# Kernel tuning notes

Hardware: AMD Instinct MI355X
Metric: run time of the kernel (lower is better)

## Reference

```python
import jax, jax.numpy as jnp
import numpy as np

B, C, E = 4, 2048, 1024
H, D = 16, 64  # num_heads, head_size

def setup_inputs() -> dict:
    key = jax.random.key(0)
    kx, kk, kq, kv, ko = jax.random.split(key, 5)
    s = 1.0 / np.sqrt(E)
    so = 1.0 / np.sqrt(H * D)
    return {
        "x": jax.random.normal(kx, (B, C, E), dtype=jnp.float32),
        "Wk": jax.random.uniform(kk, (H * D, E), jnp.float32, -s, s),
        "Wq": jax.random.uniform(kq, (H * D, E), jnp.float32, -s, s),
        "Wv": jax.random.uniform(kv, (H * D, E), jnp.float32, -s, s),
        "Wo": jax.random.uniform(ko, (E, H * D), jnp.float32, -so, so),
    }

def reference(x, Wk, Wq, Wv, Wo):
    b, c, e = x.shape
    # projections -> [B, H, C, D]
    def proj(W):
        return (x @ W.T).reshape(b, c, H, D).transpose(0, 2, 1, 3)
    k = proj(Wk)
    q = proj(Wq)
    v = proj(Wv)
    # scores [B, H, C, C]; mask applied before scaling (as in source; -inf*scale = -inf)
    sa = jnp.einsum("bhqd,bhkd->bhqk", q, k)
    mask = ~jnp.tril(jnp.ones((c, c), dtype=bool))  # True above diagonal
    masked = jnp.where(mask, -jnp.inf, sa)
    scale = 1.0 / np.sqrt(D)
    attn = jax.nn.softmax(masked * scale, axis=-1)
    out = jnp.einsum("bhqk,bhkd->bhqd", attn, v)  # [B, H, C, D]
    flat = out.transpose(0, 2, 1, 3).reshape(b, c, H * D)
    return flat @ Wo.T
```

## Files before the change

### kernel.cpp

```cpp
#include <hip/hip_runtime.h>
#include <hip/hip_bf16.h>

typedef __bf16 bf16x8 __attribute__((ext_vector_type(8)));
typedef __bf16 bf16x4 __attribute__((ext_vector_type(4)));
typedef float f32x4 __attribute__((ext_vector_type(4)));

#define NEG_INF (-__builtin_inff())

__global__ void cvt_f32_bf16(const float* __restrict__ src, __bf16* __restrict__ dst, int n) {
    int idx = blockIdx.x * blockDim.x + threadIdx.x;
    int stride = gridDim.x * blockDim.x;
    for (int i = idx * 4; i < n; i += stride * 4) {
        float4 v = *(const float4*)(src + i);
        bf16x4 o;
        o[0] = (__bf16)v.x; o[1] = (__bf16)v.y; o[2] = (__bf16)v.z; o[3] = (__bf16)v.w;
        *(bf16x4*)(dst + i) = o;
    }
}

template <int MODE>
__launch_bounds__(256, 2)
__global__ void gemm_bt(const __bf16* __restrict__ A, const __bf16* __restrict__ Bm,
                        void* __restrict__ Out, int M, int N, int K) {
    __shared__ __bf16 As[128][72];
    __shared__ __bf16 Bs[128][72];
    const int tid = threadIdx.x;
    const int w = tid >> 6, lane = tid & 63;
    const int lr = lane & 15, lg = lane >> 4;
    const int m0 = blockIdx.y * 128, n0 = blockIdx.x * 128;
    const int wm0 = (w >> 1) * 64, wn0 = (w & 1) * 64;

    f32x4 acc[4][4] = {};

    const int srow = tid >> 3;
    const int scol = (tid & 7) * 8;
    const __bf16* Ap = A + (size_t)(m0 + srow) * K + scol;
    const __bf16* Bp = Bm + (size_t)(n0 + srow) * K + scol;

    bf16x8 ar[4], br[4];
#pragma unroll
    for (int i = 0; i < 4; ++i) {
        ar[i] = *(const bf16x8*)(Ap + (size_t)i * 32 * K);
        br[i] = *(const bf16x8*)(Bp + (size_t)i * 32 * K);
    }

    const int nt = K >> 6;
    for (int t = 0; t < nt; ++t) {
        __syncthreads();
#pragma unroll
        for (int i = 0; i < 4; ++i) {
            *(bf16x8*)&As[srow + i * 32][scol] = ar[i];
            *(bf16x8*)&Bs[srow + i * 32][scol] = br[i];
        }
        __syncthreads();
        if (t + 1 < nt) {
            const __bf16* Ap2 = Ap + (size_t)(t + 1) * 64;
            const __bf16* Bp2 = Bp + (size_t)(t + 1) * 64;
#pragma unroll
            for (int i = 0; i < 4; ++i) {
                ar[i] = *(const bf16x8*)(Ap2 + (size_t)i * 32 * K);
                br[i] = *(const bf16x8*)(Bp2 + (size_t)i * 32 * K);
            }
        }
#pragma unroll
        for (int kk = 0; kk < 2; ++kk) {
            bf16x8 af[4], bf[4];
#pragma unroll
            for (int mi = 0; mi < 4; ++mi)
                af[mi] = *(const bf16x8*)&As[wm0 + mi * 16 + lr][kk * 32 + lg * 8];
#pragma unroll
            for (int ni = 0; ni < 4; ++ni)
                bf[ni] = *(const bf16x8*)&Bs[wn0 + ni * 16 + lr][kk * 32 + lg * 8];
#pragma unroll
            for (int mi = 0; mi < 4; ++mi)
#pragma unroll
                for (int ni = 0; ni < 4; ++ni)
                    acc[mi][ni] = __builtin_amdgcn_mfma_f32_16x16x32_bf16(
                        af[mi], bf[ni], acc[mi][ni], 0, 0, 0);
        }
    }

#pragma unroll
    for (int mi = 0; mi < 4; ++mi)
#pragma unroll
        for (int ni = 0; ni < 4; ++ni)
#pragma unroll
            for (int r = 0; r < 4; ++r) {
                int m = m0 + wm0 + mi * 16 + lg * 4 + r;
                int n = n0 + wn0 + ni * 16 + lr;
                float v = acc[mi][ni][r];
                if (MODE == 0) {
                    int proj = n >> 10, nn = n & 1023;
                    int h = nn >> 6, d = nn & 63;
                    int bb = m >> 11, c = m & 2047;
                    if (proj == 2) {
                        ((__bf16*)Out)[(size_t)2 * 8388608 +
                                       ((size_t)((bb * 16 + h) * 64 + d)) * 2048 + c] = (__bf16)v;
                    } else {
                        float scale = (proj == 0) ? 0.125f : 1.0f;
                        ((__bf16*)Out)[(size_t)proj * 8388608 +
                                       ((size_t)(bb * 16 + h) * 2048 + c) * 64 + d] =
                            (__bf16)(v * scale);
                    }
                } else {
                    ((float*)Out)[(size_t)m * N + n] = v;
                }
            }
}

__device__ __forceinline__ unsigned swz(unsigned d) {
    return d ^ (((d >> 7) & 7) << 4);
}

__launch_bounds__(256, 4)
__global__ void attn_fwd(const __bf16* __restrict__ Q, const __bf16* __restrict__ K,
                         const __bf16* __restrict__ Vt, __bf16* __restrict__ Aout) {
    __shared__ char smem[40960];
    const int id = blockIdx.x;
    const int vid = (id & 7) * 128 + (id >> 3);
    const int bh = vid >> 4, pr = vid & 15;
    const int w = threadIdx.x >> 6, lane = threadIdx.x & 63;
    const int lr = lane & 15, lg = lane >> 4;
    const char* Kb  = (const char*)(K  + (size_t)bh * 2048 * 64);
    const char* Vtb = (const char*)(Vt + (size_t)bh * 64 * 2048);
    const __bf16* Qb = Q + (size_t)bh * 2048 * 64;
    const int b = bh >> 4, h = bh & 15;
    char* Pb = smem + 32768 + w * 2048;

    for (int pass = 0; pass < 2; ++pass) {
        const int qt = pass ? pr : 31 - pr;
        const int q0 = qt * 64 + w * 16;
        const int nt = qt + 1;

        bf16x8 qf[2];
#pragma unroll
        for (int kk = 0; kk < 2; ++kk)
            qf[kk] = *(const bf16x8*)&Qb[(size_t)(q0 + lr) * 64 + kk * 32 + lg * 8];

        f32x4 o[4] = {};
        float m = NEG_INF, l = 0.f;

        __syncthreads();
        {
            char* kd = smem;
            char* vd = smem + 16384;
#pragma unroll
            for (int i = 0; i < 2; ++i) {
                unsigned c = (unsigned)(w * 2 + i);
                unsigned d = c * 1024 + (unsigned)lane * 16;
                unsigned bs = swz(d);
                __builtin_amdgcn_global_load_lds(
                    (const __attribute__((address_space(1))) void*)(Kb + bs),
                    (__attribute__((address_space(3))) void*)(kd + c * 1024), 16, 0, 0);
                unsigned row = bs >> 7, colb = bs & 127;
                __builtin_amdgcn_global_load_lds(
                    (const __attribute__((address_space(1))) void*)(Vtb + (size_t)row * 4096 + colb),
                    (__attribute__((address_space(3))) void*)(vd + c * 1024), 16, 0, 0);
            }
        }

        for (int t = 0; t < nt; ++t) {
            __syncthreads();
            if (t + 1 < nt) {
                char* kd = smem + ((t + 1) & 1) * 8192;
                char* vd = smem + 16384 + ((t + 1) & 1) * 8192;
#pragma unroll
                for (int i = 0; i < 2; ++i) {
                    unsigned c = (unsigned)(w * 2 + i);
                    unsigned d = c * 1024 + (unsigned)lane * 16;
                    unsigned bs = swz(d);
                    __builtin_amdgcn_global_load_lds(
                        (const __attribute__((address_space(1))) void*)(Kb + (size_t)(t + 1) * 8192 + bs),
                        (__attribute__((address_space(3))) void*)(kd + c * 1024), 16, 0, 0);
                    unsigned row = bs >> 7, colb = bs & 127;
                    __builtin_amdgcn_global_load_lds(
                        (const __attribute__((address_space(1))) void*)(Vtb + (size_t)row * 4096 +
                                                                       (size_t)(t + 1) * 128 + colb),
                        (__attribute__((address_space(3))) void*)(vd + c * 1024), 16, 0, 0);
                }
            }
            const char* Ks = smem + (t & 1) * 8192;
            const char* Vs = smem + 16384 + (t & 1) * 8192;
            const int k0 = t * 64;

            f32x4 s[4] = {};
#pragma unroll
            for (int kk = 0; kk < 2; ++kk)
#pragma unroll
                for (int sub = 0; sub < 4; ++sub) {
                    bf16x8 kf = *(const bf16x8*)(Ks + swz((unsigned)((sub * 16 + lr) * 128 + kk * 64 + lg * 16)));
                    s[sub] = __builtin_amdgcn_mfma_f32_16x16x32_bf16(kf, qf[kk], s[sub], 0, 0, 0);
                }
            if (t == qt) {
#pragma unroll
                for (int sub = 0; sub < 4; ++sub)
#pragma unroll
                    for (int r = 0; r < 4; ++r)
                        if (k0 + sub * 16 + lg * 4 + r > q0 + lr) s[sub][r] = NEG_INF;
            }
            float mloc = NEG_INF;
#pragma unroll
            for (int sub = 0; sub < 4; ++sub)
#pragma unroll
                for (int r = 0; r < 4; ++r) mloc = fmaxf(mloc, s[sub][r]);
            mloc = fmaxf(mloc, __shfl_xor(mloc, 16));
            mloc = fmaxf(mloc, __shfl_xor(mloc, 32));
            float mnew = fmaxf(m, mloc);
            float alpha = __expf(m - mnew);
            float rs = 0.f;
#pragma unroll
            for (int sub = 0; sub < 4; ++sub)
#pragma unroll
                for (int r = 0; r < 4; ++r) {
                    float p = __expf(s[sub][r] - mnew);
                    s[sub][r] = p;
                    rs += p;
                }
            rs += __shfl_xor(rs, 16);
            rs += __shfl_xor(rs, 32);
            l = l * alpha + rs;
            m = mnew;
#pragma unroll
            for (int ni = 0; ni < 4; ++ni) o[ni] *= alpha;

#pragma unroll
            for (int sub = 0; sub < 4; ++sub) {
                bf16x4 pk;
#pragma unroll
                for (int r = 0; r < 4; ++r) pk[r] = (__bf16)s[sub][r];
                *(bf16x4*)(Pb + swz((unsigned)(lr * 128 + sub * 32 + lg * 8))) = pk;
            }
            bf16x8 pfr[2];
#pragma unroll
            for (int kk = 0; kk < 2; ++kk)
                pfr[kk] = *(const bf16x8*)(Pb + swz((unsigned)(lr * 128 + kk * 64 + lg * 16)));

#pragma unroll
            for (int kk = 0; kk < 2; ++kk)
#pragma unroll
                for (int ni = 0; ni < 4; ++ni) {
                    bf16x8 vf = *(const bf16x8*)(Vs + swz((unsigned)((ni * 16 + lr) * 128 + kk * 64 + lg * 16)));
                    o[ni] = __builtin_amdgcn_mfma_f32_16x16x32_bf16(vf, pfr[kk], o[ni], 0, 0, 0);
                }
        }

        float rinv = 1.0f / l;
#pragma unroll
        for (int ni = 0; ni < 4; ++ni) {
            bf16x4 ov;
#pragma unroll
            for (int r = 0; r < 4; ++r) ov[r] = (__bf16)(o[ni][r] * rinv);
            *(bf16x4*)&Aout[((size_t)b * 2048 + q0 + lr) * 1024 + h * 64 + ni * 16 + lg * 4] = ov;
        }
    }
}

extern "C" void kernel_launch(void* const* d_in, const int* in_sizes, int n_in,
                              void* d_out, int out_size, void* d_ws, size_t ws_size,
                              hipStream_t stream) {
    const float* x  = (const float*)d_in[0];
    const float* Wk = (const float*)d_in[1];
    const float* Wq = (const float*)d_in[2];
    const float* Wv = (const float*)d_in[3];
    const float* Wo = (const float*)d_in[4];

    char* ws = (char*)d_ws;
    __bf16* xb   = (__bf16*)(ws);
    __bf16* wqkv = (__bf16*)(ws + 16777216);
    __bf16* wo_b = (__bf16*)(ws + 23068672);
    __bf16* qkv  = (__bf16*)(ws + 25165824);
    __bf16* aout = (__bf16*)(ws + 75497472);
    float* out = (float*)d_out;

    cvt_f32_bf16<<<2048, 256, 0, stream>>>(x, xb, 8388608);
    cvt_f32_bf16<<<1024, 256, 0, stream>>>(Wq, wqkv, 1048576);
    cvt_f32_bf16<<<1024, 256, 0, stream>>>(Wk, wqkv + 1048576, 1048576);
    cvt_f32_bf16<<<1024, 256, 0, stream>>>(Wv, wqkv + 2097152, 1048576);
    cvt_f32_bf16<<<1024, 256, 0, stream>>>(Wo, wo_b, 1048576);

    gemm_bt<0><<<dim3(24, 64), 256, 0, stream>>>(xb, wqkv, qkv, 8192, 3072, 1024);
    attn_fwd<<<dim3(1024), 256, 0, stream>>>(qkv, qkv + 8388608, qkv + 16777216, aout);
    gemm_bt<1><<<dim3(8, 64), 256, 0, stream>>>(aout, wo_b, out, 8192, 1024, 1024);
}
```

Before: 192.1 us.

## Rewrite projection GEMMs as 256x256 tiles with async LDS loads and ping-pong

Replaces the 128x128 register-staged GEMM with a 512-thread, 256x256-tile kernel. It loads global memory directly into swizzled LDS through global_load_lds, double-buffers the K tiles, interleaves quarter-tile MFMA phases with barriers and setprio, and remaps block IDs into 8 groups for cache locality. The aim is more reuse per block, hiding load latency behind MFMA work, and avoiding LDS bank conflicts. In exchange it uses 128KB of LDS per block and launches far fewer blocks (128 for the output GEMM), which may underfill the 256 CUs.

```diff
diff --git a/kernel.cpp b/kernel.cpp
--- a/kernel.cpp
+++ b/kernel.cpp
@@ -6,6 +6,8 @@
 typedef float f32x4 __attribute__((ext_vector_type(4)));
 
 #define NEG_INF (-__builtin_inff())
+
+#define BAR() do { asm volatile("" ::: "memory"); __builtin_amdgcn_s_barrier(); asm volatile("" ::: "memory"); } while (0)
 
 __global__ void cvt_f32_bf16(const float* __restrict__ src, __bf16* __restrict__ dst, int n) {
     int idx = blockIdx.x * blockDim.x + threadIdx.x;
@@ -19,75 +21,118 @@
 }
 
 template <int MODE>
-__launch_bounds__(256, 2)
-__global__ void gemm_bt(const __bf16* __restrict__ A, const __bf16* __restrict__ Bm,
-                        void* __restrict__ Out, int M, int N, int K) {
-    __shared__ __bf16 As[128][72];
-    __shared__ __bf16 Bs[128][72];
+__launch_bounds__(512, 2)
+__global__ void gemm8(const __bf16* __restrict__ A, const __bf16* __restrict__ Bm,
+                      void* __restrict__ Out, int M, int N, int K) {
+    __shared__ __align__(1024) char smem[131072];
     const int tid = threadIdx.x;
     const int w = tid >> 6, lane = tid & 63;
     const int lr = lane & 15, lg = lane >> 4;
-    const int m0 = blockIdx.y * 128, n0 = blockIdx.x * 128;
-    const int wm0 = (w >> 1) * 64, wn0 = (w & 1) * 64;
-
-    f32x4 acc[4][4] = {};
-
-    const int srow = tid >> 3;
-    const int scol = (tid & 7) * 8;
-    const __bf16* Ap = A + (size_t)(m0 + srow) * K + scol;
-    const __bf16* Bp = Bm + (size_t)(n0 + srow) * K + scol;
-
-    bf16x8 ar[4], br[4];
-#pragma unroll
-    for (int i = 0; i < 4; ++i) {
-        ar[i] = *(const bf16x8*)(Ap + (size_t)i * 32 * K);
-        br[i] = *(const bf16x8*)(Bp + (size_t)i * 32 * K);
+    const int wr = w >> 2, wc = w & 3;
+
+    const int nbx = gridDim.x;
+    int id = blockIdx.y * nbx + blockIdx.x;
+    int q8 = (nbx * gridDim.y) >> 3;
+    int vid = (id & 7) * q8 + (id >> 3);
+    const int m0 = (vid / nbx) * 256, n0 = (vid % nbx) * 256;
+
+    const char* Ab = (const char*)A;
+    const char* Bb = (const char*)Bm;
+
+    f32x4 acc[8][4] = {};
+    bf16x8 af[4][2], bl[2][2], bh[2][2];
+
+    auto stage = [&](int p, int t, int buf) {
+#pragma unroll
+        for (int i = 0; i < 2; ++i) {
+            unsigned drel = (unsigned)(((p & 1) << 14) + (w * 2 + i) * 1024 + lane * 16);
+            unsigned s = drel ^ (((drel >> 7) & 7) << 4);
+            unsigned srow = s >> 7, scolb = s & 127;
+            char* dst = smem + buf * 65536 + ((p < 2) ? 0 : 32768) + drel;
+            const char* src = (p < 2)
+                ? Ab + ((size_t)(m0 + srow) * K + t * 64) * 2 + scolb
+                : Bb + ((size_t)(n0 + srow) * K + t * 64) * 2 + scolb;
+            __builtin_amdgcn_global_load_lds(
+                (const __attribute__((address_space(1))) void*)src,
+                (__attribute__((address_space(3))) void*)dst, 16, 0, 0);
+        }
+    };
+    auto lda = [&](int half, const char* base) {
+#pragma unroll
+        for (int mi = 0; mi < 4; ++mi)
+#pragma unroll
+            for (int kk = 0; kk < 2; ++kk) {
+                unsigned d = (unsigned)((wr * 128 + half * 64 + mi * 16 + lr) * 128 + kk * 64 + lg * 16);
+                af[mi][kk] = *(const bf16x8*)(base + (d ^ (((d >> 7) & 7) << 4)));
+            }
+    };
+    auto ldb = [&](bf16x8 (&bf)[2][2], int nih, const char* base) {
+#pragma unroll
+        for (int ni = 0; ni < 2; ++ni)
+#pragma unroll
+            for (int kk = 0; kk < 2; ++kk) {
+                unsigned d = (unsigned)((wc * 64 + nih * 32 + ni * 16 + lr) * 128 + kk * 64 + lg * 16);
+                bf[ni][kk] = *(const bf16x8*)(base + 32768 + (d ^ (((d >> 7) & 7) << 4)));
+            }
+    };
+    auto mma = [&](bf16x8 (&bf)[2][2], int mo, int no) {
+        __builtin_amdgcn_s_setprio(1);
+#pragma unroll
+        for (int mi = 0; mi < 4; ++mi)
+#pragma unroll
+            for (int ni = 0; ni < 2; ++ni)
+#pragma unroll
+                for (int kk = 0; kk < 2; ++kk)
+                    acc[mo + mi][no + ni] = __builtin_amdgcn_mfma_f32_16x16x32_bf16(
+                        af[mi][kk], bf[ni][kk], acc[mo + mi][no + ni], 0, 0, 0);
+        __builtin_amdgcn_s_setprio(0);
+    };
+
+    const int nt = K >> 6;
+#pragma unroll
+    for (int p = 0; p < 4; ++p) stage(p, 0, 0);
+    stage(0, 1, 1);
+    asm volatile("s_waitcnt vmcnt(2)" ::: "memory");
+    BAR();
+
+    const char* b0 = smem;
+    const char* b1 = smem + 65536;
+    for (int i = 0; i < (nt >> 1); ++i) {
+        const int T = 2 * i;
+        lda(0, b0); ldb(bl, 0, b0);
+        stage(1, T + 1, 1);
+        BAR(); mma(bl, 0, 0); BAR();
+        ldb(bh, 1, b0);
+        stage(2, T + 1, 1);
+        BAR(); mma(bh, 0, 2); BAR();
+        lda(1, b0);
+        stage(3, T + 1, 1);
+        BAR(); mma(bl, 4, 0); BAR();
+        if (T + 2 < nt) { stage(0, T + 2, 0); asm volatile("s_waitcnt vmcnt(2)" ::: "memory"); }
+        else            { asm volatile("s_waitcnt vmcnt(0)" ::: "memory"); }
+        BAR(); mma(bh, 4, 2); BAR();
+        lda(0, b1); ldb(bl, 0, b1);
+        if (T + 2 < nt) stage(1, T + 2, 0);
+        BAR(); mma(bl, 0, 0); BAR();
+        ldb(bh, 1, b1);
+        if (T + 2 < nt) stage(2, T + 2, 0);
+        BAR(); mma(bh, 0, 2); BAR();
+        lda(1, b1);
+        if (T + 2 < nt) stage(3, T + 2, 0);
+        BAR(); mma(bl, 4, 0); BAR();
+        if (T + 3 < nt) { stage(0, T + 3, 1); asm volatile("s_waitcnt vmcnt(2)" ::: "memory"); }
+        else            { asm volatile("s_waitcnt vmcnt(0)" ::: "memory"); }
+        BAR(); mma(bh, 4, 2); BAR();
     }
 
-    const int nt = K >> 6;
-    for (int t = 0; t < nt; ++t) {
-        __syncthreads();
-#pragma unroll
-        for (int i = 0; i < 4; ++i) {
-            *(bf16x8*)&As[srow + i * 32][scol] = ar[i];
-            *(bf16x8*)&Bs[srow + i * 32][scol] = br[i];
-        }
-        __syncthreads();
-        if (t + 1 < nt) {
-            const __bf16* Ap2 = Ap + (size_t)(t + 1) * 64;
-            const __bf16* Bp2 = Bp + (size_t)(t + 1) * 64;
-#pragma unroll
-            for (int i = 0; i < 4; ++i) {
-                ar[i] = *(const bf16x8*)(Ap2 + (size_t)i * 32 * K);
-                br[i] = *(const bf16x8*)(Bp2 + (size_t)i * 32 * K);
-            }
-        }
-#pragma unroll
-        for (int kk = 0; kk < 2; ++kk) {
-            bf16x8 af[4], bf[4];
-#pragma unroll
-            for (int mi = 0; mi < 4; ++mi)
-                af[mi] = *(const bf16x8*)&As[wm0 + mi * 16 + lr][kk * 32 + lg * 8];
-#pragma unroll
-            for (int ni = 0; ni < 4; ++ni)
-                bf[ni] = *(const bf16x8*)&Bs[wn0 + ni * 16 + lr][kk * 32 + lg * 8];
-#pragma unroll
-            for (int mi = 0; mi < 4; ++mi)
-#pragma unroll
-                for (int ni = 0; ni < 4; ++ni)
-                    acc[mi][ni] = __builtin_amdgcn_mfma_f32_16x16x32_bf16(
-                        af[mi], bf[ni], acc[mi][ni], 0, 0, 0);
-        }
-    }
-
-#pragma unroll
-    for (int mi = 0; mi < 4; ++mi)
+#pragma unroll
+    for (int mi = 0; mi < 8; ++mi)
 #pragma unroll
         for (int ni = 0; ni < 4; ++ni)
 #pragma unroll
             for (int r = 0; r < 4; ++r) {
-                int m = m0 + wm0 + mi * 16 + lg * 4 + r;
-                int n = n0 + wn0 + ni * 16 + lr;
+                int m = m0 + wr * 128 + mi * 16 + lg * 4 + r;
+                int n = n0 + wc * 64 + ni * 16 + lr;
                 float v = acc[mi][ni][r];
                 if (MODE == 0) {
                     int proj = n >> 10, nn = n & 1023;
@@ -278,7 +323,7 @@
     cvt_f32_bf16<<<1024, 256, 0, stream>>>(Wv, wqkv + 2097152, 1048576);
     cvt_f32_bf16<<<1024, 256, 0, stream>>>(Wo, wo_b, 1048576);
 
-    gemm_bt<0><<<dim3(24, 64), 256, 0, stream>>>(xb, wqkv, qkv, 8192, 3072, 1024);
+    gemm8<0><<<dim3(12, 32), 512, 0, stream>>>(xb, wqkv, qkv, 8192, 3072, 1024);
     attn_fwd<<<dim3(1024), 256, 0, stream>>>(qkv, qkv + 8388608, qkv + 16777216, aout);
-    gemm_bt<1><<<dim3(8, 64), 256, 0, stream>>>(aout, wo_b, out, 8192, 1024, 1024);
-}
+    gemm8<1><<<dim3(4, 32), 512, 0, stream>>>(aout, wo_b, out, 8192, 1024, 1024);
+}
```

Result: slower. 204.3 us (+6.3%).

## Use direct global-to-LDS loads, XCD-aware block remap, and raise occupancy in GEMM

Applied to the files above, without the earlier changes.

Replaces the register-staged double-buffered tile loads with global_load_lds writes straight into an unpadded 32KB shared buffer, and drops the register prefetch of the next tile. Adds a block-id remap that spreads consecutive tiles across the eight XCDs, raises launch bounds to 3 blocks per CU, and wraps the MFMA loop in s_setprio. Load and compute no longer overlap within a block, and the unpadded 128-byte row stride may cause LDS bank conflicts on the fragment reads. The remap also assumes the block count divides by eight.

```diff
diff --git a/kernel.cpp b/kernel.cpp
--- a/kernel.cpp
+++ b/kernel.cpp
@@ -19,65 +19,65 @@
 }
 
 template <int MODE>
-__launch_bounds__(256, 2)
+__launch_bounds__(256, 3)
 __global__ void gemm_bt(const __bf16* __restrict__ A, const __bf16* __restrict__ Bm,
                         void* __restrict__ Out, int M, int N, int K) {
-    __shared__ __bf16 As[128][72];
-    __shared__ __bf16 Bs[128][72];
+    __shared__ __align__(1024) char smem[32768];
     const int tid = threadIdx.x;
     const int w = tid >> 6, lane = tid & 63;
     const int lr = lane & 15, lg = lane >> 4;
-    const int m0 = blockIdx.y * 128, n0 = blockIdx.x * 128;
     const int wm0 = (w >> 1) * 64, wn0 = (w & 1) * 64;
 
+    const int nbx = gridDim.x;
+    int id = blockIdx.y * nbx + blockIdx.x;
+    int q8 = (nbx * gridDim.y) >> 3;
+    int vid = (id & 7) * q8 + (id >> 3);
+    const int m0 = (vid / nbx) * 128, n0 = (vid % nbx) * 128;
+
+    const char* Ab = (const char*)A;
+    const char* Bb = (const char*)Bm;
+
     f32x4 acc[4][4] = {};
 
-    const int srow = tid >> 3;
-    const int scol = (tid & 7) * 8;
-    const __bf16* Ap = A + (size_t)(m0 + srow) * K + scol;
-    const __bf16* Bp = Bm + (size_t)(n0 + srow) * K + scol;
-
-    bf16x8 ar[4], br[4];
-#pragma unroll
-    for (int i = 0; i < 4; ++i) {
-        ar[i] = *(const bf16x8*)(Ap + (size_t)i * 32 * K);
-        br[i] = *(const bf16x8*)(Bp + (size_t)i * 32 * K);
-    }
+    const int s_row_in_chunk = lane >> 3;
+    const int s_col16 = lane & 7;
 
     const int nt = K >> 6;
     for (int t = 0; t < nt; ++t) {
+#pragma unroll
+        for (int r = 0; r < 4; ++r) {
+            int c = w * 4 + r;
+            int row = c * 8 + s_row_in_chunk;
+            const char* srcA = Ab + ((size_t)(m0 + row) * K + t * 64) * 2 + s_col16 * 16;
+            const char* srcB = Bb + ((size_t)(n0 + row) * K + t * 64) * 2 + s_col16 * 16;
+            __builtin_amdgcn_global_load_lds(
+                (const __attribute__((address_space(1))) void*)srcA,
+                (__attribute__((address_space(3))) void*)(smem + c * 1024), 16, 0, 0);
+            __builtin_amdgcn_global_load_lds(
+                (const __attribute__((address_space(1))) void*)srcB,
+                (__attribute__((address_space(3))) void*)(smem + 16384 + c * 1024), 16, 0, 0);
+        }
         __syncthreads();
-#pragma unroll
-        for (int i = 0; i < 4; ++i) {
-            *(bf16x8*)&As[srow + i * 32][scol] = ar[i];
-            *(bf16x8*)&Bs[srow + i * 32][scol] = br[i];
-        }
-        __syncthreads();
-        if (t + 1 < nt) {
-            const __bf16* Ap2 = Ap + (size_t)(t + 1) * 64;
-            const __bf16* Bp2 = Bp + (size_t)(t + 1) * 64;
-#pragma unroll
-            for (int i = 0; i < 4; ++i) {
-                ar[i] = *(const bf16x8*)(Ap2 + (size_t)i * 32 * K);
-                br[i] = *(const bf16x8*)(Bp2 + (size_t)i * 32 * K);
-            }
-        }
+
 #pragma unroll
         for (int kk = 0; kk < 2; ++kk) {
             bf16x8 af[4], bf[4];
 #pragma unroll
             for (int mi = 0; mi < 4; ++mi)
-                af[mi] = *(const bf16x8*)&As[wm0 + mi * 16 + lr][kk * 32 + lg * 8];
+                af[mi] = *(const bf16x8*)(smem + (wm0 + mi * 16 + lr) * 128 + kk * 64 + lg * 16);
 #pragma unroll
             for (int ni = 0; ni < 4; ++ni)
-                bf[ni] = *(const bf16x8*)&Bs[wn0 + ni * 16 + lr][kk * 32 + lg * 8];
+                bf[ni] = *(const bf16x8*)(smem + 16384 + (wn0 + ni * 16 + lr) * 128 + kk * 64 + lg * 16);
+            __builtin_amdgcn_s_setprio(1);
 #pragma unroll
             for (int mi = 0; mi < 4; ++mi)
 #pragma unroll
                 for (int ni = 0; ni < 4; ++ni)
                     acc[mi][ni] = __builtin_amdgcn_mfma_f32_16x16x32_bf16(
                         af[mi], bf[ni], acc[mi][ni], 0, 0, 0);
-        }
+            __builtin_amdgcn_s_setprio(0);
+        }
+        __syncthreads();
     }
 
 #pragma unroll
```

After: 192.0 us. About the same (-0.1%).
